# Optimization experiments

Hardware: AMD Instinct MI355X
Metric: run time of the kernel (lower is better)

The kernel has to match this reference:

```python
import jax, jax.numpy as jnp
import numpy as np

DIM = 64
HID = 64
BATCH = 16384
L = DIM - 1  # number of FCNN layers (for dims 1..DIM-1)


def setup_inputs() -> dict:
    key = jax.random.key(0)
    ks = jax.random.split(key, 8)
    bound = float(np.sqrt(0.5))
    return {
        "x": jax.random.normal(ks[0], (BATCH, DIM), jnp.float32),
        "initial_param": jax.random.uniform(ks[1], (2,), jnp.float32, -bound, bound),
        # padded per-layer weights: layer l uses input columns 0..l only (masked in reference)
        "W1": jax.random.normal(ks[2], (L, L, HID), jnp.float32) * 0.1,
        "b1": jnp.zeros((L, HID), jnp.float32),
        "W2": jax.random.normal(ks[3], (L, HID, HID), jnp.float32) * 0.1,
        "b2": jnp.zeros((L, HID), jnp.float32),
        "W3": jax.random.normal(ks[4], (L, HID, 2), jnp.float32) * 0.1,
        "b3": jnp.zeros((L, 2), jnp.float32),
    }


def reference(x, initial_param, W1, b1, W2, b2, W3, b3):
    B = x.shape[0]
    # mask[l, j] = 1 if input column j is visible to layer l (layer l == FCNN(in_dim=l+1))
    mask = (jnp.arange(L)[None, :] <= jnp.arange(L)[:, None]).astype(x.dtype)  # [L, L]
    xin = x[:, :L]                                                             # [B, L]
    # all per-dim FCNNs in one batched pass (equivalent to the Python loop over x[:, :i])
    h1 = jnp.tanh(jnp.einsum('bj,ljh->blh', xin, W1 * mask[:, :, None]) + b1)  # [B, L, H]
    h2 = jnp.tanh(jnp.einsum('blh,lhk->blk', h1, W2) + b2)                     # [B, L, H]
    out = jnp.einsum('blh,lhk->blk', h2, W3) + b3                              # [B, L, 2]
    mu0 = jnp.full((B, 1), initial_param[0], x.dtype)
    a0 = jnp.full((B, 1), initial_param[1], x.dtype)
    mu = jnp.concatenate([mu0, out[..., 0]], axis=1)      # [B, DIM]
    alpha = jnp.concatenate([a0, out[..., 1]], axis=1)    # [B, DIM]
    z = (x - mu) * jnp.exp(-alpha)
    log_det = -jnp.sum(alpha, axis=1)                     # [B]
    return z[:, ::-1], log_det
```

## Files before the change

### kernel.cpp

```cpp
#include <hip/hip_runtime.h>

#define LN 63
#define BATCHN 16384

typedef __attribute__((ext_vector_type(8))) short bf16x8;
typedef __attribute__((ext_vector_type(4))) float f32x4;

__device__ __forceinline__ float fast_exp(float v) {
    return __builtin_amdgcn_exp2f(v * 1.4426950408889634f);
}
__device__ __forceinline__ float fast_tanh(float v) {
    float e = __builtin_amdgcn_exp2f(v * 2.8853900817779268f);
    return 1.0f - 2.0f * __builtin_amdgcn_rcpf(e + 1.0f);
}
__device__ __forceinline__ short f2bf(float f) {
    __bf16 h = (__bf16)f;
    return __builtin_bit_cast(short, h);
}
__device__ __forceinline__ unsigned int pk2(float a, float b) {
    return (unsigned int)(unsigned short)f2bf(a) |
           ((unsigned int)(unsigned short)f2bf(b) << 16);
}

__global__ __launch_bounds__(256) void x_cvt_kernel(
    const float* __restrict__ x, unsigned short* __restrict__ xbf)
{
    const int i = (blockIdx.x * 256 + threadIdx.x) * 4;
    const float4 v = *reinterpret_cast<const float4*>(x + i);
    ushort4 o;
    o.x = (unsigned short)f2bf(v.x);
    o.y = (unsigned short)f2bf(v.y);
    o.z = (unsigned short)f2bf(v.z);
    o.w = (unsigned short)f2bf(v.w);
    *reinterpret_cast<ushort4*>(xbf + i) = o;
}

template<int XBF>
__global__ __launch_bounds__(256, 2) void maf_main_kernel(
    const float* __restrict__ x,
    const unsigned short* __restrict__ xbf,
    const float* __restrict__ W1, const float* __restrict__ b1,
    const float* __restrict__ W2, const float* __restrict__ b2,
    const float* __restrict__ W3, const float* __restrict__ b3,
    float* __restrict__ zT,
    float* __restrict__ aT)
{
    __shared__ __align__(16) char wlds[144 * 128];

    const int t = threadIdx.x;
    const int bid = blockIdx.x;
    const int l = bid % LN;
    const int rowBase = (bid / LN) * 1024;

    {
        const int h = t >> 2, jg = t & 3;
        const int sW = jg >> 1, ehi = jg & 1;
        const int swz = (h & 7) << 4;
        #pragma unroll
        for (int p = 0; p < 4; ++p) {
            float v0, v1, v2, v3;
            {
                const int j0 = 16 * jg + 4 * p;
                v0 = (j0 + 0 <= l) ? W1[(l * LN + j0 + 0) * 64 + h] : 0.0f;
                v1 = (j0 + 1 <= l) ? W1[(l * LN + j0 + 1) * 64 + h] : 0.0f;
                v2 = (j0 + 2 <= l) ? W1[(l * LN + j0 + 2) * 64 + h] : 0.0f;
                v3 = (j0 + 3 <= l) ? W1[(l * LN + j0 + 3) * 64 + h]
                                   : ((j0 + 3 == 63) ? b1[l * 64 + h] : 0.0f);
                *reinterpret_cast<uint2*>(wlds + h * 128 + ((32 * jg + 8 * p) ^ swz)) =
                    make_uint2(pk2(v0, v1), pk2(v2, v3));
            }
            {
                const int j0 = 16 * jg + 4 * p;
                v0 = W2[(l * 64 + j0 + 0) * 64 + h];
                v1 = W2[(l * 64 + j0 + 1) * 64 + h];
                v2 = W2[(l * 64 + j0 + 2) * 64 + h];
                v3 = W2[(l * 64 + j0 + 3) * 64 + h];
                *reinterpret_cast<uint2*>(wlds + (64 + h) * 128 +
                                          ((64 * sW + 16 * p + 8 * ehi) ^ swz)) =
                    make_uint2(pk2(v0, v1), pk2(v2, v3));
            }
        }
    }
    if (t < 224) {
        *reinterpret_cast<uint2*>(wlds + (130 + (t >> 4)) * 128 + (t & 15) * 8) =
            make_uint2(0u, 0u);
    }
    if (t < 128) {
        const int r = t >> 6, j = t & 63;
        const float v = W3[(l * 64 + j) * 2 + r];
        const int gj = (j >> 2) & 3, qj = j & 3, sj = j >> 5, ej = (j >> 4) & 1;
        *reinterpret_cast<unsigned short*>(
            wlds + (128 + r) * 128 +
            ((64 * sj + 16 * gj + 8 * ej + 2 * qj) ^ ((r & 7) << 4))) =
            (unsigned short)f2bf(v);
    }
    __syncthreads();

    const int lane = t & 63;
    const int w = t >> 6;
    const int g = lane >> 4;
    const int mcol = lane & 15;

    bf16x8 w1f[2][4], w2f[2][4], w3f[2];
    #pragma unroll
    for (int s = 0; s < 2; ++s) {
        const int kb = 64 * s + 16 * g;
        #pragma unroll
        for (int tt = 0; tt < 4; ++tt) {
            const int r1 = tt * 16 + mcol;
            const int r2 = 64 + tt * 16 + mcol;
            w1f[s][tt] = *reinterpret_cast<const bf16x8*>(wlds + r1 * 128 + (kb ^ ((r1 & 7) << 4)));
            w2f[s][tt] = *reinterpret_cast<const bf16x8*>(wlds + r2 * 128 + (kb ^ ((r2 & 7) << 4)));
        }
        const int r3 = 128 + mcol;
        w3f[s] = *reinterpret_cast<const bf16x8*>(wlds + r3 * 128 + (kb ^ ((r3 & 7) << 4)));
    }
    f32x4 bias2[4];
    #pragma unroll
    for (int tt = 0; tt < 4; ++tt) {
        const float4 v2 = *reinterpret_cast<const float4*>(&b2[l * 64 + 16 * tt + 4 * g]);
        bias2[tt] = f32x4{v2.x, v2.y, v2.z, v2.w};
    }
    const float b30 = b3[l * 2 + 0];
    const float b31 = b3[l * 2 + 1];
    const short one_bf = (short)0x3F80;

    #pragma unroll 2
    for (int grp = 0; grp < 16; ++grp) {
        const int row = rowBase + w * 256 + grp * 16 + mcol;

        bf16x8 xf[2];
        if constexpr (XBF) {
            xf[0] = *reinterpret_cast<const bf16x8*>(xbf + (size_t)row * 64 + 8 * g);
            xf[1] = *reinterpret_cast<const bf16x8*>(xbf + (size_t)row * 64 + 32 + 8 * g);
        } else {
            const float* xr = x + (size_t)row * 64;
            #pragma unroll
            for (int s = 0; s < 2; ++s) {
                const float4 a = *reinterpret_cast<const float4*>(xr + 32 * s + 8 * g);
                const float4 b = *reinterpret_cast<const float4*>(xr + 32 * s + 8 * g + 4);
                bf16x8 f;
                f[0] = f2bf(a.x); f[1] = f2bf(a.y); f[2] = f2bf(a.z); f[3] = f2bf(a.w);
                f[4] = f2bf(b.x); f[5] = f2bf(b.y); f[6] = f2bf(b.z); f[7] = f2bf(b.w);
                xf[s] = f;
            }
        }
        if (g == 3) xf[1][7] = one_bf;

        f32x4 c1[4];
        #pragma unroll
        for (int tt = 0; tt < 4; ++tt) c1[tt] = f32x4{0.0f, 0.0f, 0.0f, 0.0f};
        #pragma unroll
        for (int s = 0; s < 2; ++s)
            #pragma unroll
            for (int tt = 0; tt < 4; ++tt)
                c1[tt] = __builtin_amdgcn_mfma_f32_16x16x32_bf16(w1f[s][tt], xf[s], c1[tt], 0, 0, 0);

        bf16x8 pf[2];
        #pragma unroll
        for (int s = 0; s < 2; ++s) {
            bf16x8 f;
            #pragma unroll
            for (int q = 0; q < 4; ++q) {
                f[q]     = f2bf(fast_tanh(c1[2 * s][q]));
                f[4 + q] = f2bf(fast_tanh(c1[2 * s + 1][q]));
            }
            pf[s] = f;
        }

        f32x4 c2[4];
        #pragma unroll
        for (int tt = 0; tt < 4; ++tt) c2[tt] = bias2[tt];
        #pragma unroll
        for (int s = 0; s < 2; ++s)
            #pragma unroll
            for (int tt = 0; tt < 4; ++tt)
                c2[tt] = __builtin_amdgcn_mfma_f32_16x16x32_bf16(w2f[s][tt], pf[s], c2[tt], 0, 0, 0);

        bf16x8 qf[2];
        #pragma unroll
        for (int s = 0; s < 2; ++s) {
            bf16x8 f;
            #pragma unroll
            for (int q = 0; q < 4; ++q) {
                f[q]     = f2bf(fast_tanh(c2[2 * s][q]));
                f[4 + q] = f2bf(fast_tanh(c2[2 * s + 1][q]));
            }
            qf[s] = f;
        }

        f32x4 c3 = {0.0f, 0.0f, 0.0f, 0.0f};
        c3 = __builtin_amdgcn_mfma_f32_16x16x32_bf16(w3f[0], qf[0], c3, 0, 0, 0);
        c3 = __builtin_amdgcn_mfma_f32_16x16x32_bf16(w3f[1], qf[1], c3, 0, 0, 0);

        if (g == 0) {
            const float mu = c3[0] + b30;
            const float al = c3[1] + b31;
            const float xn = x[(size_t)row * 64 + l + 1];
            const float zv = (xn - mu) * fast_exp(-al);
            zT[(62 - l) * BATCHN + row] = zv;
            aT[l * BATCHN + row] = al;
        }
    }

    #pragma unroll
    for (int s = 0; s < 2; ++s) {
        #pragma unroll
        for (int tt = 0; tt < 4; ++tt) asm volatile("" :: "v"(w2f[s][tt]));
        asm volatile("" :: "v"(w3f[s]));
    }
    #pragma unroll
    for (int tt = 0; tt < 4; ++tt) asm volatile("" :: "v"(bias2[tt]));
}

__global__ __launch_bounds__(256) void maf_finish_kernel(
    const float* __restrict__ x,
    const float* __restrict__ ip,
    const float* __restrict__ ws,
    float* __restrict__ z_out,
    float* __restrict__ ld_out)
{
    const float* zT = ws;
    const float* aT = ws + (size_t)LN * BATCHN;
    __shared__ float tile[64][65];

    const int t = threadIdx.x;
    const int rb = blockIdx.x * 64;
    const float mu0 = ip[0];
    const float a0  = ip[1];
    const float e0  = fast_exp(-a0);

    {
        const int r = t >> 2, c = t & 3;
        const int row = rb + r;
        float s = 0.0f;
        for (int i = c; i < LN; i += 4) s += aT[(size_t)i * BATCHN + row];
        s += __shfl_xor(s, 1, 64);
        s += __shfl_xor(s, 2, 64);
        if (c == 0) ld_out[row] = -(s + a0);
    }

    const int r = t & 63, cq = t >> 6;
    #pragma unroll
    for (int k = 0; k < 16; ++k) {
        const int c = cq * 16 + k;
        float v;
        if (c < 63) v = zT[(size_t)c * BATCHN + rb + r];
        else        v = (x[(size_t)(rb + r) * 64] - mu0) * e0;
        tile[c][r] = v;
    }
    __syncthreads();
    #pragma unroll
    for (int i = 0; i < 16; ++i) {
        const int rr = cq * 16 + i;
        z_out[(size_t)(rb + rr) * 64 + r] = tile[r][rr];
    }
}

extern "C" void kernel_launch(void* const* d_in, const int* in_sizes, int n_in,
                              void* d_out, int out_size, void* d_ws, size_t ws_size,
                              hipStream_t stream) {
    const float* x  = (const float*)d_in[0];
    const float* ip = (const float*)d_in[1];
    const float* W1 = (const float*)d_in[2];
    const float* b1 = (const float*)d_in[3];
    const float* W2 = (const float*)d_in[4];
    const float* b2 = (const float*)d_in[5];
    const float* W3 = (const float*)d_in[6];
    const float* b3 = (const float*)d_in[7];

    float* z_out  = (float*)d_out;
    float* ld_out = z_out + (size_t)BATCHN * 64;
    float* zT = (float*)d_ws;
    float* aT = zT + (size_t)LN * BATCHN;
    unsigned short* xbf = (unsigned short*)(aT + (size_t)LN * BATCHN);

    const size_t need = (size_t)LN * BATCHN * 8 + (size_t)BATCHN * 64 * 2;
    if (ws_size >= need) {
        x_cvt_kernel<<<dim3(BATCHN * 64 / 1024), dim3(256), 0, stream>>>(x, xbf);
        maf_main_kernel<1><<<dim3(LN * 16), dim3(256), 0, stream>>>(
            x, xbf, W1, b1, W2, b2, W3, b3, zT, aT);
    } else {
        maf_main_kernel<0><<<dim3(LN * 16), dim3(256), 0, stream>>>(
            x, xbf, W1, b1, W2, b2, W3, b3, zT, aT);
    }
    maf_finish_kernel<<<dim3(BATCHN / 64), dim3(256), 0, stream>>>(
        x, ip, (const float*)d_ws, z_out, ld_out);
}
```

Measured before the change: 67.53 us.

## Precompute per-layer MFMA weight fragments in a prep kernel instead of per-block LDS staging

Adds a prep kernel that converts W1/b1, W2 and W3 once per layer into bf16 MFMA fragment order in workspace, fused with the x-to-bf16 conversion. The main kernel's 1008 blocks then load their register fragments directly with coalesced 16-byte reads. This removes the redundant per-block fp32 weight gather, bf16 conversion, LDS writes and barrier, which were repeated 16 times per layer. It drops the asm register pins, needs more workspace, and the fallback path still runs the prep kernel whether or not the workspace is large enough for it.

```diff
diff --git a/kernel.cpp b/kernel.cpp
--- a/kernel.cpp
+++ b/kernel.cpp
@@ -22,98 +22,127 @@
            ((unsigned int)(unsigned short)f2bf(b) << 16);
 }
 
-__global__ __launch_bounds__(256) void x_cvt_kernel(
-    const float* __restrict__ x, unsigned short* __restrict__ xbf)
+__device__ __forceinline__ int kappa_j(int s, int g, int e) {
+    return (e < 4) ? (32 * s + 4 * g + e) : (32 * s + 16 + 4 * g + e - 4);
+}
+
+__global__ __launch_bounds__(256) void prep_kernel(
+    const float* __restrict__ x,
+    const float* __restrict__ W1, const float* __restrict__ b1,
+    const float* __restrict__ W2, const float* __restrict__ W3,
+    unsigned short* __restrict__ Afrag,
+    unsigned short* __restrict__ xbf)
 {
-    const int i = (blockIdx.x * 256 + threadIdx.x) * 4;
-    const float4 v = *reinterpret_cast<const float4*>(x + i);
-    ushort4 o;
-    o.x = (unsigned short)f2bf(v.x);
-    o.y = (unsigned short)f2bf(v.y);
-    o.z = (unsigned short)f2bf(v.z);
-    o.w = (unsigned short)f2bf(v.w);
-    *reinterpret_cast<ushort4*>(xbf + i) = o;
+    const int t = threadIdx.x;
+    const int b = blockIdx.x;
+    if (b >= LN) {
+        const int i = ((b - LN) * 256 + t) * 4;
+        const float4 v = *reinterpret_cast<const float4*>(x + i);
+        ushort4 o;
+        o.x = (unsigned short)f2bf(v.x);
+        o.y = (unsigned short)f2bf(v.y);
+        o.z = (unsigned short)f2bf(v.z);
+        o.w = (unsigned short)f2bf(v.w);
+        *reinterpret_cast<ushort4*>(xbf + i) = o;
+        return;
+    }
+    const int l = b;
+    unsigned short* Af = Afrag + (size_t)l * 9216;
+
+    #pragma unroll
+    for (int it = 0; it < 2; ++it) {
+        const int item = t + it * 256;
+        const int s = item >> 8, tt = (item >> 6) & 3, lane = item & 63;
+        const int g = lane >> 4, mcol = lane & 15, h = 16 * tt + mcol;
+        unsigned pk[4];
+        #pragma unroll
+        for (int ep = 0; ep < 4; ++ep) {
+            float v[2];
+            #pragma unroll
+            for (int k = 0; k < 2; ++k) {
+                const int e = 2 * ep + k;
+                const int j = 32 * s + 8 * g + e;
+                float val;
+                if (j == 63)      val = b1[l * 64 + h];
+                else if (j <= l)  val = W1[(l * LN + j) * 64 + h];
+                else              val = 0.0f;
+                v[k] = val;
+            }
+            pk[ep] = pk2(v[0], v[1]);
+        }
+        *reinterpret_cast<uint4*>(Af + ((size_t)item) * 8) =
+            uint4{pk[0], pk[1], pk[2], pk[3]};
+    }
+    #pragma unroll
+    for (int it = 0; it < 2; ++it) {
+        const int item = t + it * 256;
+        const int s = item >> 8, tt = (item >> 6) & 3, lane = item & 63;
+        const int g = lane >> 4, mcol = lane & 15, h = 16 * tt + mcol;
+        unsigned pk[4];
+        #pragma unroll
+        for (int ep = 0; ep < 4; ++ep) {
+            float v[2];
+            #pragma unroll
+            for (int k = 0; k < 2; ++k) {
+                const int e = 2 * ep + k;
+                v[k] = W2[(l * 64 + kappa_j(s, g, e)) * 64 + h];
+            }
+            pk[ep] = pk2(v[0], v[1]);
+        }
+        *reinterpret_cast<uint4*>(Af + 4096 + ((size_t)item) * 8) =
+            uint4{pk[0], pk[1], pk[2], pk[3]};
+    }
+    if (t < 128) {
+        const int s = t >> 6, lane = t & 63;
+        const int g = lane >> 4, mcol = lane & 15;
+        unsigned pk[4] = {0u, 0u, 0u, 0u};
+        if (mcol < 2) {
+            #pragma unroll
+            for (int ep = 0; ep < 4; ++ep) {
+                float v[2];
+                #pragma unroll
+                for (int k = 0; k < 2; ++k) {
+                    const int e = 2 * ep + k;
+                    v[k] = W3[(l * 64 + kappa_j(s, g, e)) * 2 + mcol];
+                }
+                pk[ep] = pk2(v[0], v[1]);
+            }
+        }
+        *reinterpret_cast<uint4*>(Af + 8192 + ((size_t)t) * 8) =
+            uint4{pk[0], pk[1], pk[2], pk[3]};
+    }
 }
 
 template<int XBF>
 __global__ __launch_bounds__(256, 2) void maf_main_kernel(
     const float* __restrict__ x,
     const unsigned short* __restrict__ xbf,
-    const float* __restrict__ W1, const float* __restrict__ b1,
-    const float* __restrict__ W2, const float* __restrict__ b2,
-    const float* __restrict__ W3, const float* __restrict__ b3,
+    const unsigned short* __restrict__ Afrag,
+    const float* __restrict__ b2,
+    const float* __restrict__ b3,
     float* __restrict__ zT,
     float* __restrict__ aT)
 {
-    __shared__ __align__(16) char wlds[144 * 128];
-
     const int t = threadIdx.x;
     const int bid = blockIdx.x;
     const int l = bid % LN;
     const int rowBase = (bid / LN) * 1024;
 
-    {
-        const int h = t >> 2, jg = t & 3;
-        const int sW = jg >> 1, ehi = jg & 1;
-        const int swz = (h & 7) << 4;
-        #pragma unroll
-        for (int p = 0; p < 4; ++p) {
-            float v0, v1, v2, v3;
-            {
-                const int j0 = 16 * jg + 4 * p;
-                v0 = (j0 + 0 <= l) ? W1[(l * LN + j0 + 0) * 64 + h] : 0.0f;
-                v1 = (j0 + 1 <= l) ? W1[(l * LN + j0 + 1) * 64 + h] : 0.0f;
-                v2 = (j0 + 2 <= l) ? W1[(l * LN + j0 + 2) * 64 + h] : 0.0f;
-                v3 = (j0 + 3 <= l) ? W1[(l * LN + j0 + 3) * 64 + h]
-                                   : ((j0 + 3 == 63) ? b1[l * 64 + h] : 0.0f);
-                *reinterpret_cast<uint2*>(wlds + h * 128 + ((32 * jg + 8 * p) ^ swz)) =
-                    make_uint2(pk2(v0, v1), pk2(v2, v3));
-            }
-            {
-                const int j0 = 16 * jg + 4 * p;
-                v0 = W2[(l * 64 + j0 + 0) * 64 + h];
-                v1 = W2[(l * 64 + j0 + 1) * 64 + h];
-                v2 = W2[(l * 64 + j0 + 2) * 64 + h];
-                v3 = W2[(l * 64 + j0 + 3) * 64 + h];
-                *reinterpret_cast<uint2*>(wlds + (64 + h) * 128 +
-                                          ((64 * sW + 16 * p + 8 * ehi) ^ swz)) =
-                    make_uint2(pk2(v0, v1), pk2(v2, v3));
-            }
-        }
-    }
-    if (t < 224) {
-        *reinterpret_cast<uint2*>(wlds + (130 + (t >> 4)) * 128 + (t & 15) * 8) =
-            make_uint2(0u, 0u);
-    }
-    if (t < 128) {
-        const int r = t >> 6, j = t & 63;
-        const float v = W3[(l * 64 + j) * 2 + r];
-        const int gj = (j >> 2) & 3, qj = j & 3, sj = j >> 5, ej = (j >> 4) & 1;
-        *reinterpret_cast<unsigned short*>(
-            wlds + (128 + r) * 128 +
-            ((64 * sj + 16 * gj + 8 * ej + 2 * qj) ^ ((r & 7) << 4))) =
-            (unsigned short)f2bf(v);
-    }
-    __syncthreads();
-
     const int lane = t & 63;
     const int w = t >> 6;
     const int g = lane >> 4;
     const int mcol = lane & 15;
 
+    const unsigned short* Af = Afrag + (size_t)l * 9216;
     bf16x8 w1f[2][4], w2f[2][4], w3f[2];
     #pragma unroll
     for (int s = 0; s < 2; ++s) {
-        const int kb = 64 * s + 16 * g;
         #pragma unroll
         for (int tt = 0; tt < 4; ++tt) {
-            const int r1 = tt * 16 + mcol;
-            const int r2 = 64 + tt * 16 + mcol;
-            w1f[s][tt] = *reinterpret_cast<const bf16x8*>(wlds + r1 * 128 + (kb ^ ((r1 & 7) << 4)));
-            w2f[s][tt] = *reinterpret_cast<const bf16x8*>(wlds + r2 * 128 + (kb ^ ((r2 & 7) << 4)));
-        }
-        const int r3 = 128 + mcol;
-        w3f[s] = *reinterpret_cast<const bf16x8*>(wlds + r3 * 128 + (kb ^ ((r3 & 7) << 4)));
+            w1f[s][tt] = *reinterpret_cast<const bf16x8*>(Af + ((s * 4 + tt) * 64 + lane) * 8);
+            w2f[s][tt] = *reinterpret_cast<const bf16x8*>(Af + 4096 + ((s * 4 + tt) * 64 + lane) * 8);
+        }
+        w3f[s] = *reinterpret_cast<const bf16x8*>(Af + 8192 + (s * 64 + lane) * 8);
     }
     f32x4 bias2[4];
     #pragma unroll
@@ -202,26 +231,16 @@
             aT[l * BATCHN + row] = al;
         }
     }
-
-    #pragma unroll
-    for (int s = 0; s < 2; ++s) {
-        #pragma unroll
-        for (int tt = 0; tt < 4; ++tt) asm volatile("" :: "v"(w2f[s][tt]));
-        asm volatile("" :: "v"(w3f[s]));
-    }
-    #pragma unroll
-    for (int tt = 0; tt < 4; ++tt) asm volatile("" :: "v"(bias2[tt]));
 }
 
 __global__ __launch_bounds__(256) void maf_finish_kernel(
     const float* __restrict__ x,
     const float* __restrict__ ip,
-    const float* __restrict__ ws,
+    const float* __restrict__ zT,
+    const float* __restrict__ aT,
     float* __restrict__ z_out,
     float* __restrict__ ld_out)
 {
-    const float* zT = ws;
-    const float* aT = ws + (size_t)LN * BATCHN;
     __shared__ float tile[64][65];
 
     const int t = threadIdx.x;
@@ -271,19 +290,25 @@
 
     float* z_out  = (float*)d_out;
     float* ld_out = z_out + (size_t)BATCHN * 64;
-    float* zT = (float*)d_ws;
+
+    unsigned short* Afrag = (unsigned short*)d_ws;
+    float* zT = (float*)((char*)d_ws + (size_t)LN * 9216 * 2);
     float* aT = zT + (size_t)LN * BATCHN;
     unsigned short* xbf = (unsigned short*)(aT + (size_t)LN * BATCHN);
 
-    const size_t need = (size_t)LN * BATCHN * 8 + (size_t)BATCHN * 64 * 2;
-    if (ws_size >= need) {
-        x_cvt_kernel<<<dim3(BATCHN * 64 / 1024), dim3(256), 0, stream>>>(x, xbf);
+    const size_t need_xbf = (size_t)LN * 9216 * 2 + (size_t)LN * BATCHN * 8 +
+                            (size_t)BATCHN * 64 * 2;
+    if (ws_size >= need_xbf) {
+        prep_kernel<<<dim3(LN + BATCHN * 64 / 1024), dim3(256), 0, stream>>>(
+            x, W1, b1, W2, W3, Afrag, xbf);
         maf_main_kernel<1><<<dim3(LN * 16), dim3(256), 0, stream>>>(
-            x, xbf, W1, b1, W2, b2, W3, b3, zT, aT);
+            x, xbf, Afrag, b2, b3, zT, aT);
     } else {
+        prep_kernel<<<dim3(LN), dim3(256), 0, stream>>>(
+            x, W1, b1, W2, W3, Afrag, xbf);
         maf_main_kernel<0><<<dim3(LN * 16), dim3(256), 0, stream>>>(
-            x, xbf, W1, b1, W2, b2, W3, b3, zT, aT);
+            x, xbf, Afrag, b2, b3, zT, aT);
     }
     maf_finish_kernel<<<dim3(BATCHN / 64), dim3(256), 0, stream>>>(
-        x, ip, (const float*)d_ws, z_out, ld_out);
-}
+        x, ip, zT, aT, z_out, ld_out);
+}
```

New measurement: 66.16 us. 2.0% less time.
